# Kernel optimization log

Hardware: AMD Instinct MI355X
Metric: run time of the kernel (lower is better)

The kernel has to match this reference:

```python
import jax, jax.numpy as jnp
import numpy as np

B, S, DMODEL, HEADS = 2, 2048, 1024, 16
DK = DMODEL // HEADS
DV = DMODEL // HEADS


def setup_inputs() -> dict:
    key = jax.random.key(0)
    kx, kq, kk, kv = jax.random.split(key, 4)
    x = jax.random.normal(kx, (B, S, DMODEL), dtype=jnp.float32)
    # stacked per-head projection weights, shape [H, dmodel, dk/dv]
    # (equivalent to nn.Linear(dmodel, dk, bias=False) per head)
    scale = 1.0 / np.sqrt(DMODEL)
    Wq = jax.random.uniform(kq, (HEADS, DMODEL, DK), jnp.float32, -scale, scale)
    Wk = jax.random.uniform(kk, (HEADS, DMODEL, DK), jnp.float32, -scale, scale)
    Wv = jax.random.uniform(kv, (HEADS, DMODEL, DV), jnp.float32, -scale, scale)
    return {"x": x, "Wq": Wq, "Wk": Wk, "Wv": Wv}


def reference(x, Wq, Wk, Wv):
    # per-head projections, batched across heads: [B,H,S,dk]
    q = jnp.einsum("bsd,hdk->bhsk", x, Wq)
    k = jnp.einsum("bsd,hdk->bhsk", x, Wk)
    v = jnp.einsum("bsd,hdv->bhsv", x, Wv)
    # NOTE: original module applies NO 1/sqrt(dk) scaling — keep faithful
    scores = jnp.einsum("bhqk,bhsk->bhqs", q, k)  # [B,H,S,S]
    attn = jax.nn.softmax(scores, axis=-1)
    out = jnp.einsum("bhqs,bhsv->bhqv", attn, v)  # [B,H,S,dv]
    # concat heads along last dim in head order
    Bsz, H, Sq, Dv = out.shape
    return jnp.transpose(out, (0, 2, 1, 3)).reshape(Bsz, Sq, H * Dv)
```

## Files before the change

### kernel.cpp

```cpp
#include <hip/hip_runtime.h>

#define B_ 2
#define S_ 2048
#define D_ 1024
#define H_ 16
#define DK_ 64
#define M_ (B_ * S_)
#define N_ (3 * D_)

typedef __bf16 bf16x8 __attribute__((ext_vector_type(8)));
typedef short s8vec __attribute__((ext_vector_type(8)));
typedef float f4vec __attribute__((ext_vector_type(4)));

static __device__ __forceinline__ ushort f2b(float f) {
  union { float f; unsigned u; } v; v.f = f;
  unsigned u = v.u;
  u += 0x7FFFu + ((u >> 16) & 1u);
  return (ushort)(u >> 16);
}

static __device__ __forceinline__ unsigned pk2(float a, float b) {
#if __has_builtin(__builtin_amdgcn_cvt_pk_bf16_f32)
  typedef __bf16 b2 __attribute__((ext_vector_type(2)));
  b2 r = __builtin_amdgcn_cvt_pk_bf16_f32(a, b);
  return __builtin_bit_cast(unsigned, r);
#else
  return (unsigned)f2b(a) | ((unsigned)f2b(b) << 16);
#endif
}

static __device__ __forceinline__ float fexp2(float x) {
#if __has_builtin(__builtin_amdgcn_exp2f)
  return __builtin_amdgcn_exp2f(x);
#else
  return exp2f(x);
#endif
}

static __device__ __forceinline__ f4vec mfma16(s8vec a, s8vec b, f4vec c) {
  return __builtin_amdgcn_mfma_f32_16x16x32_bf16(
      __builtin_bit_cast(bf16x8, a), __builtin_bit_cast(bf16x8, b), c, 0, 0, 0);
}

static __device__ __forceinline__ void gl_lds16(const ushort* g, ushort* l) {
  __builtin_amdgcn_global_load_lds(
      (const __attribute__((address_space(1))) unsigned*)g,
      (__attribute__((address_space(3))) unsigned*)l, 16, 0, 0);
}

static __device__ __forceinline__ void wg_barrier_lds() {
  asm volatile("" ::: "memory");
  __builtin_amdgcn_s_waitcnt(0xC07F);
  __builtin_amdgcn_s_barrier();
  asm volatile("" ::: "memory");
}

__global__ __launch_bounds__(256) void cvt_all(const float* __restrict__ x,
                                               const float* __restrict__ Wq,
                                               const float* __restrict__ Wk,
                                               const float* __restrict__ Wv,
                                               ushort* __restrict__ xb,
                                               ushort* __restrict__ wbt) {
  const int t = threadIdx.x;
  if (blockIdx.x < 4096) {
    int i = blockIdx.x * 256 + t;
    float4 v = ((const float4*)x)[i];
    ushort4 o;
    o.x = f2b(v.x); o.y = f2b(v.y); o.z = f2b(v.z); o.w = f2b(v.w);
    ((ushort4*)xb)[i] = o;
  } else {
    __shared__ ushort T[64 * 72];
    int bid = blockIdx.x - 4096;
    int w = bid >> 8, rem = bid & 255;
    int h = rem >> 4, d0 = (rem & 15) * 64;
    const float* W = (w == 0) ? Wq : (w == 1) ? Wk : Wv;
    const float* src = W + (size_t)h * 65536 + (size_t)d0 * 64;
#pragma unroll
    for (int j = 0; j < 4; ++j) {
      int idx = j * 256 + t;
      int dr = idx >> 4, kc = (idx & 15) * 4;
      float4 v = *(const float4*)(src + dr * 64 + kc);
      T[(kc + 0) * 72 + dr] = f2b(v.x);
      T[(kc + 1) * 72 + dr] = f2b(v.y);
      T[(kc + 2) * 72 + dr] = f2b(v.z);
      T[(kc + 3) * 72 + dr] = f2b(v.w);
    }
    __syncthreads();
    const int kk = t >> 2, dcg = (t & 3) * 16;
    ushort* dst = wbt + ((size_t)w * 1024 + h * 64 + kk) * 1024 + d0 + dcg;
    *(s8vec*)dst       = *(const s8vec*)&T[kk * 72 + dcg];
    *(s8vec*)(dst + 8) = *(const s8vec*)&T[kk * 72 + dcg + 8];
  }
}

__global__ __launch_bounds__(256) void proj_gemm(const ushort* __restrict__ xb,
                                                 const ushort* __restrict__ wbt,
                                                 ushort* __restrict__ qkv) {
  __shared__ __attribute__((aligned(16))) ushort BUF[2 * 128 * 64];
  ushort* As = BUF;
  ushort* Bs = BUF + 128 * 64;
  const int tid = threadIdx.x, wid = tid >> 6, lane = tid & 63;
  const int quad = lane >> 4, l15 = lane & 15;
  const int wm = wid & 1, wn = wid >> 1;
  const int m0 = blockIdx.x * 128, n0 = blockIdx.y * 128;

  f4vec acc[4][4];
#pragma unroll
  for (int mb = 0; mb < 4; mb++)
#pragma unroll
    for (int nb = 0; nb < 4; nb++)
#pragma unroll
      for (int i = 0; i < 4; i++) acc[mb][nb][i] = 0.f;

  const int sr = tid >> 3, sg = tid & 7;
  const int lg = sg ^ (sr & 7);
  const ushort* Ab = xb + (size_t)m0 * D_;
  const ushort* Bb = wbt + (size_t)n0 * D_;

  for (int k0 = 0; k0 < D_; k0 += 64) {
    __syncthreads();
#pragma unroll
    for (int j = 0; j < 4; ++j) {
      int r = j * 32 + sr;
      gl_lds16(Ab + (size_t)r * D_ + k0 + lg * 8, &As[j * 2048 + wid * 512]);
      gl_lds16(Bb + (size_t)r * D_ + k0 + lg * 8, &Bs[j * 2048 + wid * 512]);
    }
    __syncthreads();

#pragma unroll
    for (int kb = 0; kb < 2; ++kb) {
      s8vec af[4], bf[4];
#pragma unroll
      for (int mb = 0; mb < 4; ++mb) {
        int m = wm * 64 + mb * 16 + l15;
        int gpos = (kb * 4 + quad) ^ (m & 7);
        af[mb] = *(const s8vec*)&As[m * 64 + gpos * 8];
      }
#pragma unroll
      for (int nb = 0; nb < 4; ++nb) {
        int n = wn * 64 + nb * 16 + l15;
        int gpos = (kb * 4 + quad) ^ (n & 7);
        bf[nb] = *(const s8vec*)&Bs[n * 64 + gpos * 8];
      }
#pragma unroll
      for (int mb = 0; mb < 4; ++mb)
#pragma unroll
        for (int nb = 0; nb < 4; ++nb)
          acc[mb][nb] = mfma16(af[mb], bf[nb], acc[mb][nb]);
    }
  }

  __syncthreads();
  ushort* T = BUF + wid * 4096;
  const size_t per = (size_t)B_ * H_ * S_ * DK_;
  const int w = n0 >> 10;
  const int sb = m0 + wm * 64;
  const int b = sb >> 11;
  const int nb0 = (n0 & 1023) + wn * 64;

  if (w == 2) {
#pragma unroll
    for (int mb = 0; mb < 4; ++mb) {
      const int mc = mb * 2 + (quad >> 1);
      const int moff = (quad & 1) * 4;
#pragma unroll
      for (int nb = 0; nb < 4; ++nb) {
        const int np = nb * 16 + l15;
        unsigned p01 = pk2(acc[mb][nb][0], acc[mb][nb][1]);
        unsigned p23 = pk2(acc[mb][nb][2], acc[mb][nb][3]);
        *(uint2*)&T[np * 64 + ((mc ^ (np & 7)) * 8) + moff] = make_uint2(p01, p23);
      }
    }
    ushort* vt = qkv + 2 * per;
#pragma unroll
    for (int j = 0; j < 8; ++j) {
      const int np = (lane >> 3) + j * 8;
      const int mc2 = lane & 7;
      s8vec v = *(const s8vec*)&T[np * 64 + ((mc2 ^ (np & 7)) * 8)];
      const int n1 = nb0 + np;
      *(s8vec*)(vt + ((size_t)b * 1024 + n1) * S_ + (sb & 2047) + mc2 * 8) = v;
    }
  } else {
    const float qs = (w == 0) ? 1.44269504f : 1.0f;
#pragma unroll
    for (int mb = 0; mb < 4; ++mb)
#pragma unroll
      for (int nb = 0; nb < 4; ++nb) {
        const int c = nb * 2 + (l15 >> 3);
#pragma unroll
        for (int i = 0; i < 4; ++i) {
          const int mp = mb * 16 + quad * 4 + i;
          T[mp * 64 + ((c ^ (mp & 7)) * 8) + (l15 & 7)] = f2b(acc[mb][nb][i] * qs);
        }
      }
    const int h = nb0 >> 6;
    ushort* qk = qkv + (size_t)w * per + (((size_t)b * H_ + h) * S_) * 64;
#pragma unroll
    for (int j = 0; j < 8; ++j) {
      const int mp = (lane >> 3) + j * 8;
      const int c2 = lane & 7;
      s8vec v = *(const s8vec*)&T[mp * 64 + ((c2 ^ (mp & 7)) * 8)];
      *(s8vec*)(qk + (size_t)((sb & 2047) + mp) * 64 + c2 * 8) = v;
    }
  }
}

__global__ __launch_bounds__(128) void attn(const ushort* __restrict__ qg,
                                            const ushort* __restrict__ kg,
                                            const ushort* __restrict__ vtg,
                                            float* __restrict__ out) {
  __shared__ __attribute__((aligned(16))) ushort Ks[64 * 64];
  __shared__ __attribute__((aligned(16))) ushort Vt[80 * 64];
  __shared__ __attribute__((aligned(16))) ushort Ps[2][32 * 64];
  const int qt = blockIdx.x, bh = blockIdx.y;
  const int b = bh >> 4, h = bh & 15;
  const int tid = threadIdx.x, wid = tid >> 6, lane = tid & 63;
  const int quad = lane >> 4, l15 = lane & 15, l7 = l15 & 7;

  {
    ushort* p = &Vt[(64 + (tid >> 3)) * 64 + (tid & 7) * 8];
#pragma unroll
    for (int j = 0; j < 8; ++j) p[j] = 0x3F80;
  }

  const ushort* qbase = qg + ((size_t)bh * S_ + qt * 64 + wid * 32) * DK_;
  s8vec aq[2][2];
#pragma unroll
  for (int mb = 0; mb < 2; mb++) {
    aq[mb][0] = *(const s8vec*)(qbase + (size_t)(mb * 16 + l15) * DK_ + quad * 8);
    aq[mb][1] = *(const s8vec*)(qbase + (size_t)(mb * 16 + l15) * DK_ + 32 + quad * 8);
  }

  f4vec o[2][5];
#pragma unroll
  for (int mb = 0; mb < 2; mb++)
#pragma unroll
    for (int nb = 0; nb < 5; nb++)
#pragma unroll
      for (int i = 0; i < 4; i++) o[mb][nb][i] = 0.f;

  const int r0 = tid >> 3, gs = tid & 7;
  const int gk = gs ^ (r0 & 7);
  const ushort* kb_ = kg + (size_t)bh * S_ * DK_;
  const ushort* vb_ = vtg + (size_t)bh * 64 * S_;

  s8vec kpre[4], vpre[4];
#pragma unroll
  for (int j = 0; j < 4; ++j) {
    kpre[j] = *(const s8vec*)(kb_ + (size_t)(j * 16 + r0) * DK_ + gk * 8);
    vpre[j] = *(const s8vec*)(vb_ + (size_t)(j * 16 + r0) * S_ + gk * 8);
  }

  for (int kt = 0; kt < S_ / 64; ++kt) {
    wg_barrier_lds();
#pragma unroll
    for (int j = 0; j < 4; ++j) {
      *(s8vec*)&Ks[(j * 16 + r0) * 64 + gs * 8] = kpre[j];
      *(s8vec*)&Vt[(j * 16 + r0) * 64 + gs * 8] = vpre[j];
    }
    if (kt + 1 < S_ / 64) {
      const ushort* kn = kb_ + (size_t)((kt + 1) * 64 + r0) * DK_ + gk * 8;
      const ushort* vn = vb_ + (size_t)r0 * S_ + (kt + 1) * 64 + gk * 8;
#pragma unroll
      for (int j = 0; j < 4; ++j) {
        kpre[j] = *(const s8vec*)(kn + (size_t)(j * 16) * DK_);
        vpre[j] = *(const s8vec*)(vn + (size_t)(j * 16) * S_);
      }
    }
    wg_barrier_lds();

    f4vec sct[2][4];
#pragma unroll
    for (int nb = 0; nb < 4; nb++) {
      const int row = nb * 16 + l15;
      s8vec ak0 = *(const s8vec*)&Ks[row * 64 + ((0 + quad) ^ l7) * 8];
      s8vec ak1 = *(const s8vec*)&Ks[row * 64 + ((4 + quad) ^ l7) * 8];
#pragma unroll
      for (int mb = 0; mb < 2; mb++) {
        f4vec z;
#pragma unroll
        for (int i = 0; i < 4; i++) z[i] = 0.f;
        z = mfma16(ak0, aq[mb][0], z);
        sct[mb][nb] = mfma16(ak1, aq[mb][1], z);
      }
    }

#pragma unroll
    for (int mb = 0; mb < 2; mb++) {
      const int q = mb * 16 + l15;
#pragma unroll
      for (int nb = 0; nb < 4; nb++) {
        f4vec p;
#pragma unroll
        for (int i = 0; i < 4; i++) p[i] = fexp2(sct[mb][nb][i]);
        unsigned p01 = pk2(p[0], p[1]);
        unsigned p23 = pk2(p[2], p[3]);
        const int c = (nb * 2 + (quad >> 1)) ^ l7;
        *(uint2*)&Ps[wid][q * 64 + c * 8 + (quad & 1) * 4] = make_uint2(p01, p23);
      }
    }

#pragma unroll
    for (int kc = 0; kc < 2; kc++) {
      s8vec ap[2];
#pragma unroll
      for (int mb = 0; mb < 2; mb++)
        ap[mb] = *(const s8vec*)&Ps[wid][(mb * 16 + l15) * 64 + ((kc * 4 + quad) ^ l7) * 8];
#pragma unroll
      for (int nb = 0; nb < 5; nb++) {
        s8vec av = *(const s8vec*)&Vt[(nb * 16 + l15) * 64 + ((kc * 4 + quad) ^ l7) * 8];
        o[0][nb] = mfma16(av, ap[0], o[0][nb]);
        o[1][nb] = mfma16(av, ap[1], o[1][nb]);
      }
    }
  }

#pragma unroll
  for (int mb = 0; mb < 2; mb++) {
    const float inv = 1.0f / o[mb][4][0];
    float* ob = out + ((size_t)b * S_ + qt * 64 + wid * 32 + mb * 16 + l15) * D_ + h * DK_;
#pragma unroll
    for (int nb = 0; nb < 4; nb++) {
      float4 v;
      v.x = o[mb][nb][0] * inv;
      v.y = o[mb][nb][1] * inv;
      v.z = o[mb][nb][2] * inv;
      v.w = o[mb][nb][3] * inv;
      *(float4*)(ob + nb * 16 + quad * 4) = v;
    }
  }
}

extern "C" void kernel_launch(void* const* d_in, const int* in_sizes, int n_in,
                              void* d_out, int out_size, void* d_ws, size_t ws_size,
                              hipStream_t stream) {
  const float* x  = (const float*)d_in[0];
  const float* Wq = (const float*)d_in[1];
  const float* Wk = (const float*)d_in[2];
  const float* Wv = (const float*)d_in[3];
  float* out = (float*)d_out;

  ushort* qkv = (ushort*)d_ws;
  const size_t per = (size_t)B_ * H_ * S_ * DK_;
  ushort* xb  = qkv + 3 * per;
  ushort* wbt = xb + (size_t)B_ * S_ * D_;

  cvt_all<<<4096 + 768, 256, 0, stream>>>(x, Wq, Wk, Wv, xb, wbt);
  proj_gemm<<<dim3(M_ / 128, N_ / 128), 256, 0, stream>>>(xb, wbt, qkv);
  attn<<<dim3(S_ / 64, B_ * H_), 128, 0, stream>>>(qkv, qkv + per, qkv + 2 * per, out);
}
```

Baseline: 183.9 us.

## Restructure attention to 128-query blocks of 8 waves with 128-key tiles

The attention kernel moves from 2 waves × 32 queries per block over 64-key tiles to 8 waves × 16 queries per block over 128-key tiles. Each K/V tile loaded into LDS is now shared by 128 queries instead of 64, which halves global K/V traffic and the number of barrier iterations per key. The cost is fewer blocks (512 instead of 1024), more LDS per block, and less register-level reuse per wave, since each wave now holds one query row-block instead of two.

After: 176.0 us. -4.3%, faster.

```diff
diff --git a/kernel.cpp b/kernel.cpp
--- a/kernel.cpp
+++ b/kernel.cpp
@@ -205,129 +205,103 @@
   }
 }
 
-__global__ __launch_bounds__(128) void attn(const ushort* __restrict__ qg,
+__global__ __launch_bounds__(512) void attn(const ushort* __restrict__ qg,
                                             const ushort* __restrict__ kg,
                                             const ushort* __restrict__ vtg,
                                             float* __restrict__ out) {
-  __shared__ __attribute__((aligned(16))) ushort Ks[64 * 64];
-  __shared__ __attribute__((aligned(16))) ushort Vt[80 * 64];
-  __shared__ __attribute__((aligned(16))) ushort Ps[2][32 * 64];
+  __shared__ __attribute__((aligned(16))) ushort Ks[128 * 64];
+  __shared__ __attribute__((aligned(16))) ushort Vt[80 * 128];
+  __shared__ __attribute__((aligned(16))) ushort Ps[8][16 * 128];
   const int qt = blockIdx.x, bh = blockIdx.y;
   const int b = bh >> 4, h = bh & 15;
   const int tid = threadIdx.x, wid = tid >> 6, lane = tid & 63;
   const int quad = lane >> 4, l15 = lane & 15, l7 = l15 & 7;
 
-  {
-    ushort* p = &Vt[(64 + (tid >> 3)) * 64 + (tid & 7) * 8];
+  if (tid < 256) {
+    ushort* p = &Vt[(64 + (tid >> 4)) * 128 + (tid & 15) * 8];
 #pragma unroll
     for (int j = 0; j < 8; ++j) p[j] = 0x3F80;
   }
 
-  const ushort* qbase = qg + ((size_t)bh * S_ + qt * 64 + wid * 32) * DK_;
-  s8vec aq[2][2];
-#pragma unroll
-  for (int mb = 0; mb < 2; mb++) {
-    aq[mb][0] = *(const s8vec*)(qbase + (size_t)(mb * 16 + l15) * DK_ + quad * 8);
-    aq[mb][1] = *(const s8vec*)(qbase + (size_t)(mb * 16 + l15) * DK_ + 32 + quad * 8);
-  }
-
-  f4vec o[2][5];
-#pragma unroll
-  for (int mb = 0; mb < 2; mb++)
-#pragma unroll
-    for (int nb = 0; nb < 5; nb++)
-#pragma unroll
-      for (int i = 0; i < 4; i++) o[mb][nb][i] = 0.f;
-
-  const int r0 = tid >> 3, gs = tid & 7;
-  const int gk = gs ^ (r0 & 7);
+  const ushort* qbase = qg + ((size_t)bh * S_ + qt * 128 + wid * 16) * DK_;
+  s8vec aq0 = *(const s8vec*)(qbase + (size_t)l15 * DK_ + quad * 8);
+  s8vec aq1 = *(const s8vec*)(qbase + (size_t)l15 * DK_ + 32 + quad * 8);
+
+  f4vec o[5];
+#pragma unroll
+  for (int nb = 0; nb < 5; nb++)
+#pragma unroll
+    for (int i = 0; i < 4; i++) o[nb][i] = 0.f;
+
+  const int r = tid >> 3, gs = tid & 7;
+  const int gk = gs ^ (r & 7);
+  const int rv = tid >> 4, cs = tid & 15;
+  const int gv = (cs & 8) | ((cs & 7) ^ (rv & 7));
   const ushort* kb_ = kg + (size_t)bh * S_ * DK_;
   const ushort* vb_ = vtg + (size_t)bh * 64 * S_;
 
-  s8vec kpre[4], vpre[4];
-#pragma unroll
-  for (int j = 0; j < 4; ++j) {
-    kpre[j] = *(const s8vec*)(kb_ + (size_t)(j * 16 + r0) * DK_ + gk * 8);
-    vpre[j] = *(const s8vec*)(vb_ + (size_t)(j * 16 + r0) * S_ + gk * 8);
-  }
-
-  for (int kt = 0; kt < S_ / 64; ++kt) {
+  s8vec kpre[2], vpre[2];
+  kpre[0] = *(const s8vec*)(kb_ + (size_t)r * DK_ + gk * 8);
+  kpre[1] = *(const s8vec*)(kb_ + (size_t)(r + 64) * DK_ + gk * 8);
+  vpre[0] = *(const s8vec*)(vb_ + (size_t)rv * S_ + gv * 8);
+  vpre[1] = *(const s8vec*)(vb_ + (size_t)(rv + 32) * S_ + gv * 8);
+
+  for (int kt = 0; kt < S_ / 128; ++kt) {
     wg_barrier_lds();
-#pragma unroll
-    for (int j = 0; j < 4; ++j) {
-      *(s8vec*)&Ks[(j * 16 + r0) * 64 + gs * 8] = kpre[j];
-      *(s8vec*)&Vt[(j * 16 + r0) * 64 + gs * 8] = vpre[j];
-    }
-    if (kt + 1 < S_ / 64) {
-      const ushort* kn = kb_ + (size_t)((kt + 1) * 64 + r0) * DK_ + gk * 8;
-      const ushort* vn = vb_ + (size_t)r0 * S_ + (kt + 1) * 64 + gk * 8;
-#pragma unroll
-      for (int j = 0; j < 4; ++j) {
-        kpre[j] = *(const s8vec*)(kn + (size_t)(j * 16) * DK_);
-        vpre[j] = *(const s8vec*)(vn + (size_t)(j * 16) * S_);
-      }
+    *(s8vec*)&Ks[r * 64 + gs * 8]          = kpre[0];
+    *(s8vec*)&Ks[(r + 64) * 64 + gs * 8]   = kpre[1];
+    *(s8vec*)&Vt[rv * 128 + cs * 8]        = vpre[0];
+    *(s8vec*)&Vt[(rv + 32) * 128 + cs * 8] = vpre[1];
+    if (kt + 1 < S_ / 128) {
+      const ushort* kn = kb_ + (size_t)((kt + 1) * 128 + r) * DK_ + gk * 8;
+      kpre[0] = *(const s8vec*)(kn);
+      kpre[1] = *(const s8vec*)(kn + (size_t)64 * DK_);
+      const ushort* vn = vb_ + (size_t)rv * S_ + (kt + 1) * 128 + gv * 8;
+      vpre[0] = *(const s8vec*)(vn);
+      vpre[1] = *(const s8vec*)(vn + (size_t)32 * S_);
     }
     wg_barrier_lds();
 
-    f4vec sct[2][4];
-#pragma unroll
-    for (int nb = 0; nb < 4; nb++) {
+#pragma unroll
+    for (int nb = 0; nb < 8; nb++) {
       const int row = nb * 16 + l15;
       s8vec ak0 = *(const s8vec*)&Ks[row * 64 + ((0 + quad) ^ l7) * 8];
       s8vec ak1 = *(const s8vec*)&Ks[row * 64 + ((4 + quad) ^ l7) * 8];
-#pragma unroll
-      for (int mb = 0; mb < 2; mb++) {
-        f4vec z;
-#pragma unroll
-        for (int i = 0; i < 4; i++) z[i] = 0.f;
-        z = mfma16(ak0, aq[mb][0], z);
-        sct[mb][nb] = mfma16(ak1, aq[mb][1], z);
-      }
-    }
-
-#pragma unroll
-    for (int mb = 0; mb < 2; mb++) {
-      const int q = mb * 16 + l15;
-#pragma unroll
-      for (int nb = 0; nb < 4; nb++) {
-        f4vec p;
-#pragma unroll
-        for (int i = 0; i < 4; i++) p[i] = fexp2(sct[mb][nb][i]);
-        unsigned p01 = pk2(p[0], p[1]);
-        unsigned p23 = pk2(p[2], p[3]);
-        const int c = (nb * 2 + (quad >> 1)) ^ l7;
-        *(uint2*)&Ps[wid][q * 64 + c * 8 + (quad & 1) * 4] = make_uint2(p01, p23);
-      }
-    }
-
-#pragma unroll
-    for (int kc = 0; kc < 2; kc++) {
-      s8vec ap[2];
-#pragma unroll
-      for (int mb = 0; mb < 2; mb++)
-        ap[mb] = *(const s8vec*)&Ps[wid][(mb * 16 + l15) * 64 + ((kc * 4 + quad) ^ l7) * 8];
+      f4vec z;
+#pragma unroll
+      for (int i = 0; i < 4; i++) z[i] = 0.f;
+      z = mfma16(ak0, aq0, z);
+      z = mfma16(ak1, aq1, z);
+      f4vec p;
+#pragma unroll
+      for (int i = 0; i < 4; i++) p[i] = fexp2(z[i]);
+      unsigned p01 = pk2(p[0], p[1]);
+      unsigned p23 = pk2(p[2], p[3]);
+      const int c = (nb * 2 + (quad >> 1)) ^ l7;
+      *(uint2*)&Ps[wid][l15 * 128 + c * 8 + (quad & 1) * 4] = make_uint2(p01, p23);
+    }
+
+#pragma unroll
+    for (int kc = 0; kc < 4; kc++) {
+      s8vec ap = *(const s8vec*)&Ps[wid][l15 * 128 + ((kc * 4 + quad) ^ l7) * 8];
 #pragma unroll
       for (int nb = 0; nb < 5; nb++) {
-        s8vec av = *(const s8vec*)&Vt[(nb * 16 + l15) * 64 + ((kc * 4 + quad) ^ l7) * 8];
-        o[0][nb] = mfma16(av, ap[0], o[0][nb]);
-        o[1][nb] = mfma16(av, ap[1], o[1][nb]);
-      }
-    }
-  }
-
-#pragma unroll
-  for (int mb = 0; mb < 2; mb++) {
-    const float inv = 1.0f / o[mb][4][0];
-    float* ob = out + ((size_t)b * S_ + qt * 64 + wid * 32 + mb * 16 + l15) * D_ + h * DK_;
-#pragma unroll
-    for (int nb = 0; nb < 4; nb++) {
-      float4 v;
-      v.x = o[mb][nb][0] * inv;
-      v.y = o[mb][nb][1] * inv;
-      v.z = o[mb][nb][2] * inv;
-      v.w = o[mb][nb][3] * inv;
-      *(float4*)(ob + nb * 16 + quad * 4) = v;
-    }
+        s8vec av = *(const s8vec*)&Vt[(nb * 16 + l15) * 128 + ((kc * 4 + quad) ^ l7) * 8];
+        o[nb] = mfma16(av, ap, o[nb]);
+      }
+    }
+  }
+
+  const float inv = 1.0f / o[4][0];
+  float* ob = out + ((size_t)b * S_ + qt * 128 + wid * 16 + l15) * D_ + h * DK_;
+#pragma unroll
+  for (int nb = 0; nb < 4; nb++) {
+    float4 v;
+    v.x = o[nb][0] * inv;
+    v.y = o[nb][1] * inv;
+    v.z = o[nb][2] * inv;
+    v.w = o[nb][3] * inv;
+    *(float4*)(ob + nb * 16 + quad * 4) = v;
   }
 }
 
@@ -347,5 +321,5 @@
 
   cvt_all<<<4096 + 768, 256, 0, stream>>>(x, Wq, Wk, Wv, xb, wbt);
   proj_gemm<<<dim3(M_ / 128, N_ / 128), 256, 0, stream>>>(xb, wbt, qkv);
-  attn<<<dim3(S_ / 64, B_ * H_), 128, 0, stream>>>(qkv, qkv + per, qkv + 2 * per, out);
-}
+  attn<<<dim3(S_ / 128, B_ * H_), 512, 0, stream>>>(qkv, qkv + per, qkv + 2 * per, out);
+}
```
